# Optimization experiments

Hardware: AMD Instinct MI355X
Metric: run time of the kernel (lower is better)

Reference implementation:

```python
import math
import jax, jax.numpy as jnp
import numpy as np

HIDDEN = 2048
N_HEAD = 16
HEAD_DIM = HIDDEN // N_HEAD
LAYER_NUMBER = 1  # max(1, layer_number)
NORM_FACTOR = math.sqrt(HEAD_DIM) * LAYER_NUMBER


def build_alibi(seq_len, n_head):
    # n_head is a power of 2 -> slopes_i = 2^(-8*(i+1)/n_head)  (ALiBi paper)
    slopes = 2.0 ** (-8.0 * jnp.arange(1, n_head + 1, dtype=jnp.float32) / n_head)
    pos = jnp.arange(seq_len, dtype=jnp.float32)
    return slopes[:, None, None] * pos[None, None, :]  # (n_head, 1, seq_len)


def setup_inputs() -> dict:
    key = jax.random.key(0)
    ks = jax.random.split(key, 6)
    B, S = 2, 2048
    hidden_states = jax.random.normal(ks[0], (B, S, HIDDEN), jnp.float32)
    residual = jax.random.normal(ks[1], (B, S, HIDDEN), jnp.float32)
    attention_mask = jnp.ones((B, S), jnp.float32)  # no padding
    W_qkv = jax.random.normal(ks[2], (3 * HIDDEN, HIDDEN), jnp.float32) * (1.0 / math.sqrt(HIDDEN))
    b_qkv = jax.random.normal(ks[3], (3 * HIDDEN,), jnp.float32) * 0.02
    W_dense = jax.random.normal(ks[4], (HIDDEN, HIDDEN), jnp.float32) * (1.0 / math.sqrt(HIDDEN))
    b_dense = jax.random.normal(ks[5], (HIDDEN,), jnp.float32) * 0.02
    return {"hidden_states": hidden_states, "residual": residual,
            "attention_mask": attention_mask, "W_qkv": W_qkv, "b_qkv": b_qkv,
            "W_dense": W_dense, "b_dense": b_dense}


def reference(hidden_states, residual, attention_mask, W_qkv, b_qkv, W_dense, b_dense):
    B, S, H = hidden_states.shape
    nh, hd = N_HEAD, HEAD_DIM

    # fused QKV projection; split_tensor_along_last_dim over the per-head 3*hd axis
    mixed = hidden_states @ W_qkv.T + b_qkv              # [B,S,3H]
    mixed = mixed.reshape(B, S, nh, 3, hd)
    q = mixed[..., 0, :]                                  # [B,S,nh,hd]
    k = mixed[..., 1, :]
    v = mixed[..., 2, :]

    # baddbmm: beta*alibi + alpha*(q @ k^T)
    alibi = build_alibi(S, nh)                            # (nh,1,S)
    beta = 1.0 / LAYER_NUMBER
    alpha = 1.0 / NORM_FACTOR
    scores = alpha * jnp.einsum('bqnd,bknd->bnqk', q, k) + beta * alibi[None]  # [B,nh,S,S]

    # BloomScaledSoftmax: scale by layer_number, apply padded causal mask,
    # softmax in fp32, zero out masked probs
    scores = scores * LAYER_NUMBER
    mask_bool = attention_mask == 0.0                     # [B,S] True where padded
    causal = jnp.tril(jnp.ones((S, S), dtype=bool))       # [S,S]
    padded = (mask_bool[:, None, :, None]                 # query side
              | (~causal)[None, None]                     # causal
              | mask_bool[:, None, None, :])              # key side -> [B,1,S,S]
    scores = jnp.where(padded, jnp.float32(-10000.0), scores)
    probs = jax.nn.softmax(scores.astype(jnp.float32), axis=-1) * (~padded)
    probs = probs.astype(v.dtype)

    # attention_dropout/hidden_dropout are identity in eval mode
    context = jnp.einsum('bnqk,bknd->bqnd', probs, v).reshape(B, S, H)
    out = context @ W_dense.T + b_dense                   # dense (skip_bias_add folded)
    return residual + out
```

## Files before the change

kernel.cpp:

```cpp
#include <hip/hip_runtime.h>
#include <math.h>

#define HIDDEN 2048
#define NHEAD 16
#define HD 128
#define SEQ 2048
#define BATCH 2
#define MROWS (BATCH * SEQ)
#define K3 (3 * HIDDEN)

#define SCORE_SCALE 0.08838834764831845f

using short8 = __attribute__((ext_vector_type(8))) short;
using f32x4 = __attribute__((ext_vector_type(4))) float;

__device__ __forceinline__ unsigned short f2bf(float f) {
  union { float f; unsigned int u; } v; v.f = f;
  const unsigned int u = v.u;
  return (unsigned short)((u + 0x7FFFu + ((u >> 16) & 1u)) >> 16);
}

__device__ __forceinline__ void gl2lds16(const void* g, void* l) {
#pragma clang diagnostic push
#pragma clang diagnostic ignored "-Waddress-space-conversion"
  __builtin_amdgcn_global_load_lds(
      (const __attribute__((address_space(1))) unsigned int*)g,
      (__attribute__((address_space(3))) unsigned int*)l, 16, 0, 0);
#pragma clang diagnostic pop
}

__global__ __launch_bounds__(256) void cvt_all(
    const float* __restrict__ s0, unsigned short* __restrict__ d0, int n0,
    const float* __restrict__ s1, unsigned short* __restrict__ d1, int n1,
    const float* __restrict__ s2, unsigned short* __restrict__ d2, int n2) {
  int i = (blockIdx.x * 256 + threadIdx.x) * 8;
  const float* src;
  unsigned short* dst;
  if (i < n0) {
    src = s0; dst = d0;
  } else if (i < n0 + n1) {
    src = s1; dst = d1; i -= n0;
  } else {
    src = s2; dst = d2; i -= n0 + n1;
    if (i >= n2) return;
  }
  const float4 a = *(const float4*)(src + i);
  const float4 b = *(const float4*)(src + i + 4);
  ushort4 oa, ob;
  oa.x = f2bf(a.x); oa.y = f2bf(a.y); oa.z = f2bf(a.z); oa.w = f2bf(a.w);
  ob.x = f2bf(b.x); ob.y = f2bf(b.y); ob.z = f2bf(b.z); ob.w = f2bf(b.w);
  *(ushort4*)(dst + i) = oa;
  *(ushort4*)(dst + i + 4) = ob;
}

template <int MODE>
__global__ __launch_bounds__(256) void gemm_mfma(
    const unsigned short* __restrict__ A, const unsigned short* __restrict__ W,
    const float* __restrict__ bias, const float* __restrict__ residual,
    unsigned short* __restrict__ q, unsigned short* __restrict__ k,
    unsigned short* __restrict__ v, float* __restrict__ outf, int K) {
  __shared__ __align__(16) unsigned short As[128 * 32];
  __shared__ __align__(16) unsigned short Bs[128 * 32];
  const int tid = threadIdx.x;
  const int lane = tid & 63;
  const int wave = tid >> 6;
  const int l15 = lane & 15;
  const int quad = lane >> 4;
  const int wr = wave >> 1, wc = wave & 1;
  const int m0 = blockIdx.y << 7;
  const int n0 = blockIdx.x << 7;

  f32x4 acc[4][4];
#pragma unroll
  for (int i = 0; i < 4; ++i)
#pragma unroll
    for (int j = 0; j < 4; ++j) {
      f32x4 z = {0.f, 0.f, 0.f, 0.f};
      acc[i][j] = z;
    }

  const int kg0 = tid >> 7, mr0 = tid & 127;
  const int kg1 = (tid + 256) >> 7, mr1 = tid & 127;

  for (int k0 = 0; k0 < K; k0 += 32) {
    gl2lds16(A + (size_t)(m0 + mr0) * K + k0 + kg0 * 8, (char*)As + tid * 16);
    gl2lds16(W + (size_t)(n0 + mr0) * K + k0 + kg0 * 8, (char*)Bs + tid * 16);
    gl2lds16(A + (size_t)(m0 + mr1) * K + k0 + kg1 * 8,
             (char*)As + 4096 + tid * 16);
    gl2lds16(W + (size_t)(n0 + mr1) * K + k0 + kg1 * 8,
             (char*)Bs + 4096 + tid * 16);
    __syncthreads();
    short8 af[4], bf[4];
#pragma unroll
    for (int i = 0; i < 4; ++i)
      af[i] = *(const short8*)((const char*)As + quad * 2048 +
                               (wr * 64 + i * 16 + l15) * 16);
#pragma unroll
    for (int j = 0; j < 4; ++j)
      bf[j] = *(const short8*)((const char*)Bs + quad * 2048 +
                               (wc * 64 + j * 16 + l15) * 16);
#pragma unroll
    for (int i = 0; i < 4; ++i)
#pragma unroll
      for (int j = 0; j < 4; ++j)
        acc[i][j] =
            __builtin_amdgcn_mfma_f32_16x16x32_bf16(af[i], bf[j], acc[i][j],
                                                    0, 0, 0);
    __syncthreads();
  }

  if (MODE == 0) {
#pragma unroll
    for (int i = 0; i < 4; ++i) {
#pragma unroll
      for (int j = 0; j < 4; ++j) {
        const int n = n0 + wc * 64 + j * 16 + l15;
        const float bi = bias[n];
        const int h = n / 384;
        const int rem = n - h * 384;
        const int which = rem >> 7;
        const int d = rem & 127;
        const int mb = m0 + wr * 64 + i * 16 + quad * 4;
        const int bb = mb >> 11, ssb = mb & 2047;
        const int bh = (bb << 4) + h;
        if (which == 2) {
          const int dt = d >> 4, dl = d & 15;
          const int ksup = ssb >> 5, ntl = (ssb >> 4) & 1, qq = (ssb >> 2) & 3;
          ushort4 pk;
          pk.x = f2bf(acc[i][j][0] + bi);
          pk.y = f2bf(acc[i][j][1] + bi);
          pk.z = f2bf(acc[i][j][2] + bi);
          pk.w = f2bf(acc[i][j][3] + bi);
          *(ushort4*)(v +
                      ((((size_t)(bh * 8 + dt) * (SEQ / 32) + ksup) * 4 + qq) *
                       16 + dl) * 8 + ntl * 4) = pk;
        } else {
          unsigned short* dst = (which == 0) ? q : k;
#pragma unroll
          for (int p = 0; p < 4; ++p)
            dst[((size_t)(bh << 11) + ssb + p) * HD + d] =
                f2bf(acc[i][j][p] + bi);
        }
      }
    }
  } else {
#pragma unroll
    for (int i = 0; i < 4; ++i) {
#pragma unroll
      for (int j = 0; j < 4; ++j) {
        const int n = n0 + wc * 64 + j * 16 + l15;
        const float bi = bias[n];
#pragma unroll
        for (int p = 0; p < 4; ++p) {
          const int m = m0 + wr * 64 + i * 16 + quad * 4 + p;
          outf[(size_t)m * HIDDEN + n] =
              acc[i][j][p] + bi + residual[(size_t)m * HIDDEN + n];
        }
      }
    }
  }
}

__global__ __launch_bounds__(256) void attn_mfma3(
    const unsigned short* __restrict__ qb, const unsigned short* __restrict__ kb,
    const unsigned short* __restrict__ vt4, unsigned short* __restrict__ ctx) {
  __shared__ __align__(16) unsigned short Ks[8192];
  __shared__ __align__(16) unsigned short Vs[8192];

  const int tid = threadIdx.x;
  const int lane = tid & 63;
  const int w = tid >> 6;
  const int l15 = lane & 15;
  const int quad = lane >> 4;
  const int bt = gridDim.x - 1 - blockIdx.x;
  const int q0 = bt << 6;
  const int h = blockIdx.y, b = blockIdx.z;
  const int bh = b * NHEAD + h;
  const float slope = exp2f(-0.5f * (float)(h + 1));
  const unsigned short* qp = qb + ((size_t)bh * SEQ + q0 + w * 16) * HD;
  const unsigned short* kp = kb + (size_t)bh * SEQ * HD;
  const unsigned short* vp = vt4 + (size_t)bh * SEQ * HD;

  short8 qf[4];
#pragma unroll
  for (int dt = 0; dt < 4; ++dt)
    qf[dt] = *(const short8*)(qp + (size_t)l15 * HD + dt * 32 + quad * 8);

  f32x4 O[8];
#pragma unroll
  for (int i = 0; i < 8; ++i) {
    f32x4 z = {0.f, 0.f, 0.f, 0.f};
    O[i] = z;
  }
  float mrow = -3.0e38f, lrow = 0.f;
  const int qg = q0 + w * 16 + l15;

  for (int kt = 0; kt <= bt; ++kt) {
#pragma unroll
    for (int p = 0; p < 4; ++p) {
      const int idx = tid + p * 256;
      const int reg = idx >> 6;
      const int nts = reg >> 2, dts = reg & 3;
      const int qs = (idx >> 4) & 3, ls = idx & 15;
      gl2lds16(kp + (size_t)(kt * 64 + nts * 16 + ls) * HD + dts * 32 + qs * 8,
               (char*)Ks + idx * 16);
    }
#pragma unroll
    for (int p = 0; p < 4; ++p) {
      const int idx = tid + p * 256;
      const int ntv = idx >> 7, off = idx & 127;
      gl2lds16(vp + ((size_t)(ntv * 64 + kt * 2)) * 512 + off * 8,
               (char*)Vs + idx * 16);
    }
    __syncthreads();

    f32x4 sc[4];
#pragma unroll
    for (int nt = 0; nt < 4; ++nt) {
      f32x4 z = {0.f, 0.f, 0.f, 0.f};
      sc[nt] = z;
    }
    const int ntmax = (kt == bt) ? (w + 1) : 4;
#pragma unroll
    for (int dt = 0; dt < 4; ++dt) {
#pragma unroll
      for (int nt = 0; nt < 4; ++nt) {
        if (nt < ntmax) {
          const short8 kf = *(const short8*)(
              (const char*)Ks + ((((nt * 4 + dt) * 4 + quad) * 16 + l15) << 4));
          sc[nt] = __builtin_amdgcn_mfma_f32_16x16x32_bf16(kf, qf[dt], sc[nt],
                                                           0, 0, 0);
        }
      }
    }

    const bool diag = (kt == bt);
    float pv[4][4];
    float pm = -3.0e38f;
#pragma unroll
    for (int nt = 0; nt < 4; ++nt) {
      const int kbase = kt * 64 + nt * 16 + quad * 4;
#pragma unroll
      for (int r = 0; r < 4; ++r) {
        const int kg = kbase + r;
        float s = fmaf(sc[nt][r], SCORE_SCALE, slope * (float)kg);
        if (diag && kg > qg) s = -1.0e30f;
        pv[nt][r] = s;
        pm = fmaxf(pm, s);
      }
    }
    pm = fmaxf(pm, __shfl_xor(pm, 16, 64));
    pm = fmaxf(pm, __shfl_xor(pm, 32, 64));
    const float mnew = fmaxf(mrow, pm);
    const float alpha = __expf(mrow - mnew);
    mrow = mnew;
    float rsum = 0.f;
#pragma unroll
    for (int nt = 0; nt < 4; ++nt)
#pragma unroll
      for (int r = 0; r < 4; ++r) {
        const float p = __expf(pv[nt][r] - mnew);
        pv[nt][r] = p;
        rsum += p;
      }
    rsum += __shfl_xor(rsum, 16, 64);
    rsum += __shfl_xor(rsum, 32, 64);
    lrow = lrow * alpha + rsum;

    float aO[4];
#pragma unroll
    for (int r = 0; r < 4; ++r)
      aO[r] = __shfl(alpha, (quad << 4) + (quad << 2) + r, 64);
#pragma unroll
    for (int o = 0; o < 8; ++o)
#pragma unroll
      for (int r = 0; r < 4; ++r) O[o][r] *= aO[r];

    union { short8 s; unsigned int u[4]; } pf[2];
#pragma unroll
    for (int nt = 0; nt < 4; ++nt) {
      const unsigned int lo =
          (unsigned int)f2bf(pv[nt][0]) | ((unsigned int)f2bf(pv[nt][1]) << 16);
      const unsigned int hi =
          (unsigned int)f2bf(pv[nt][2]) | ((unsigned int)f2bf(pv[nt][3]) << 16);
      pf[nt >> 1].u[(nt & 1) * 2] = lo;
      pf[nt >> 1].u[(nt & 1) * 2 + 1] = hi;
    }

#pragma unroll
    for (int s2 = 0; s2 < 2; ++s2) {
#pragma unroll
      for (int nt = 0; nt < 8; ++nt) {
        const short8 vf = *(const short8*)(
            (const char*)Vs + nt * 2048 + s2 * 1024 + quad * 256 + l15 * 16);
        O[nt] = __builtin_amdgcn_mfma_f32_16x16x32_bf16(pf[s2].s, vf, O[nt],
                                                        0, 0, 0);
      }
    }
    __syncthreads();
  }

  const float linv = 1.f / lrow;
  float iO[4];
#pragma unroll
  for (int r = 0; r < 4; ++r)
    iO[r] = __shfl(linv, (quad << 4) + (quad << 2) + r, 64);
#pragma unroll
  for (int nt = 0; nt < 8; ++nt)
#pragma unroll
    for (int r = 0; r < 4; ++r)
      ctx[((size_t)b * SEQ + q0 + w * 16 + quad * 4 + r) * HIDDEN + h * HD +
          nt * 16 + l15] = f2bf(O[nt][r] * iO[r]);
}

extern "C" void kernel_launch(void* const* d_in, const int* in_sizes, int n_in,
                              void* d_out, int out_size, void* d_ws,
                              size_t ws_size, hipStream_t stream) {
  const float* hs = (const float*)d_in[0];
  const float* res = (const float*)d_in[1];
  const float* Wqkv = (const float*)d_in[3];
  const float* bqkv = (const float*)d_in[4];
  const float* Wd = (const float*)d_in[5];
  const float* bd = (const float*)d_in[6];
  float* out = (float*)d_out;

  const size_t per = (size_t)BATCH * NHEAD * SEQ * HD;
  const size_t n_hs = (size_t)MROWS * HIDDEN;
  const size_t n_wq = (size_t)K3 * HIDDEN;
  const size_t n_wd = (size_t)HIDDEN * HIDDEN;

  unsigned short* ws = (unsigned short*)d_ws;
  unsigned short* qb = ws;
  unsigned short* kb = qb + per;
  unsigned short* vtb = kb + per;
  unsigned short* ctxb = vtb + per;
  unsigned short* hs_bf = ctxb + n_hs;
  unsigned short* wq_bf = hs_bf + n_hs;
  unsigned short* wd_bf = wq_bf + n_wq;

  dim3 blk(256);
  const unsigned cvt_blocks = (unsigned)((n_hs + n_wq + n_wd) / 8 / 256);
  cvt_all<<<dim3(cvt_blocks), blk, 0, stream>>>(
      hs, hs_bf, (int)n_hs, Wqkv, wq_bf, (int)n_wq, Wd, wd_bf, (int)n_wd);
  gemm_mfma<0><<<dim3(K3 / 128, MROWS / 128), blk, 0, stream>>>(
      hs_bf, wq_bf, bqkv, nullptr, qb, kb, vtb, nullptr, HIDDEN);
  attn_mfma3<<<dim3(SEQ / 64, NHEAD, BATCH), blk, 0, stream>>>(qb, kb, vtb,
                                                               ctxb);
  gemm_mfma<1><<<dim3(HIDDEN / 128, MROWS / 128), blk, 0, stream>>>(
      ctxb, wd_bf, bd, res, nullptr, nullptr, nullptr, out, HIDDEN);
}
```

Baseline: 600.3 us.

## Double attention query tile per block and swizzle GEMM block order

The attention kernel now handles 128 query rows per block, with each wave owning two 16-row query subtiles. Every K/V tile loaded into LDS is therefore reused for twice as many queries, halving K/V global traffic and the number of blocks. Both GEMMs switch to a 1D grid that groups blocks into 4x4 supertiles, so neighbouring blocks share A and W tiles in L2. The costs are higher register pressure from the doubled accumulators, possibly lower occupancy, and half as many attention blocks to spread across the GPU.

```diff
diff --git a/kernel.cpp b/kernel.cpp
--- a/kernel.cpp
+++ b/kernel.cpp
@@ -53,7 +53,7 @@
   *(ushort4*)(dst + i + 4) = ob;
 }
 
-template <int MODE>
+template <int MODE, int NPN>
 __global__ __launch_bounds__(256) void gemm_mfma(
     const unsigned short* __restrict__ A, const unsigned short* __restrict__ W,
     const float* __restrict__ bias, const float* __restrict__ residual,
@@ -67,8 +67,11 @@
   const int l15 = lane & 15;
   const int quad = lane >> 4;
   const int wr = wave >> 1, wc = wave & 1;
-  const int m0 = blockIdx.y << 7;
-  const int n0 = blockIdx.x << 7;
+  const int bid = blockIdx.x;
+  const int p = bid >> 4, off = bid & 15;
+  const int pr = p / NPN, pc = p % NPN;
+  const int m0 = ((pr << 2) + (off >> 2)) << 7;
+  const int n0 = ((pc << 2) + (off & 3)) << 7;
 
   f32x4 acc[4][4];
 #pragma unroll
@@ -137,9 +140,9 @@
         } else {
           unsigned short* dst = (which == 0) ? q : k;
 #pragma unroll
-          for (int p = 0; p < 4; ++p)
-            dst[((size_t)(bh << 11) + ssb + p) * HD + d] =
-                f2bf(acc[i][j][p] + bi);
+          for (int p2 = 0; p2 < 4; ++p2)
+            dst[((size_t)(bh << 11) + ssb + p2) * HD + d] =
+                f2bf(acc[i][j][p2] + bi);
         }
       }
     }
@@ -151,17 +154,17 @@
         const int n = n0 + wc * 64 + j * 16 + l15;
         const float bi = bias[n];
 #pragma unroll
-        for (int p = 0; p < 4; ++p) {
-          const int m = m0 + wr * 64 + i * 16 + quad * 4 + p;
+        for (int p2 = 0; p2 < 4; ++p2) {
+          const int m = m0 + wr * 64 + i * 16 + quad * 4 + p2;
           outf[(size_t)m * HIDDEN + n] =
-              acc[i][j][p] + bi + residual[(size_t)m * HIDDEN + n];
-        }
-      }
-    }
-  }
-}
-
-__global__ __launch_bounds__(256) void attn_mfma3(
+              acc[i][j][p2] + bi + residual[(size_t)m * HIDDEN + n];
+        }
+      }
+    }
+  }
+}
+
+__global__ __launch_bounds__(256) void attn_mfma4(
     const unsigned short* __restrict__ qb, const unsigned short* __restrict__ kb,
     const unsigned short* __restrict__ vt4, unsigned short* __restrict__ ctx) {
   __shared__ __align__(16) unsigned short Ks[8192];
@@ -173,29 +176,37 @@
   const int l15 = lane & 15;
   const int quad = lane >> 4;
   const int bt = gridDim.x - 1 - blockIdx.x;
-  const int q0 = bt << 6;
+  const int q0 = bt << 7;
   const int h = blockIdx.y, b = blockIdx.z;
   const int bh = b * NHEAD + h;
   const float slope = exp2f(-0.5f * (float)(h + 1));
-  const unsigned short* qp = qb + ((size_t)bh * SEQ + q0 + w * 16) * HD;
+  const unsigned short* qp = qb + ((size_t)bh * SEQ + q0 + w * 32) * HD;
   const unsigned short* kp = kb + (size_t)bh * SEQ * HD;
   const unsigned short* vp = vt4 + (size_t)bh * SEQ * HD;
 
-  short8 qf[4];
+  short8 qf[4][2];
 #pragma unroll
   for (int dt = 0; dt < 4; ++dt)
-    qf[dt] = *(const short8*)(qp + (size_t)l15 * HD + dt * 32 + quad * 8);
-
-  f32x4 O[8];
+#pragma unroll
+    for (int u = 0; u < 2; ++u)
+      qf[dt][u] =
+          *(const short8*)(qp + (size_t)(u * 16 + l15) * HD + dt * 32 + quad * 8);
+
+  f32x4 O0[8], O1[8];
 #pragma unroll
   for (int i = 0; i < 8; ++i) {
     f32x4 z = {0.f, 0.f, 0.f, 0.f};
-    O[i] = z;
-  }
-  float mrow = -3.0e38f, lrow = 0.f;
-  const int qg = q0 + w * 16 + l15;
-
-  for (int kt = 0; kt <= bt; ++kt) {
+    O0[i] = z;
+    O1[i] = z;
+  }
+  float mrow0 = -3.0e38f, lrow0 = 0.f;
+  float mrow1 = -3.0e38f, lrow1 = 0.f;
+  const int qlo = q0 + w * 32;
+  const int qg0 = qlo + l15, qg1 = qlo + 16 + l15;
+  const int dlim = 2 * bt + (w >> 1);
+  const int ktend = 2 * bt + 1;
+
+  for (int kt = 0; kt <= ktend; ++kt) {
 #pragma unroll
     for (int p = 0; p < 4; ++p) {
       const int idx = tid + p * 256;
@@ -214,103 +225,143 @@
     }
     __syncthreads();
 
-    f32x4 sc[4];
-#pragma unroll
-    for (int nt = 0; nt < 4; ++nt) {
-      f32x4 z = {0.f, 0.f, 0.f, 0.f};
-      sc[nt] = z;
-    }
-    const int ntmax = (kt == bt) ? (w + 1) : 4;
-#pragma unroll
-    for (int dt = 0; dt < 4; ++dt) {
+    if (kt <= dlim) {
+      const bool diag = (kt == dlim);
+      const int ntmax = diag ? ((w & 1) ? 4 : 2) : 4;
+      const int kbase = kt << 6;
+
+      f32x4 sc0[4], sc1[4];
 #pragma unroll
       for (int nt = 0; nt < 4; ++nt) {
-        if (nt < ntmax) {
-          const short8 kf = *(const short8*)(
-              (const char*)Ks + ((((nt * 4 + dt) * 4 + quad) * 16 + l15) << 4));
-          sc[nt] = __builtin_amdgcn_mfma_f32_16x16x32_bf16(kf, qf[dt], sc[nt],
-                                                           0, 0, 0);
-        }
-      }
-    }
-
-    const bool diag = (kt == bt);
-    float pv[4][4];
-    float pm = -3.0e38f;
-#pragma unroll
-    for (int nt = 0; nt < 4; ++nt) {
-      const int kbase = kt * 64 + nt * 16 + quad * 4;
+        f32x4 z = {0.f, 0.f, 0.f, 0.f};
+        sc0[nt] = z;
+        sc1[nt] = z;
+      }
+#pragma unroll
+      for (int dt = 0; dt < 4; ++dt) {
+#pragma unroll
+        for (int nt = 0; nt < 4; ++nt) {
+          if (nt < ntmax) {
+            const short8 kf = *(const short8*)(
+                (const char*)Ks +
+                ((((nt * 4 + dt) * 4 + quad) * 16 + l15) << 4));
+            sc0[nt] = __builtin_amdgcn_mfma_f32_16x16x32_bf16(kf, qf[dt][0],
+                                                              sc0[nt], 0, 0, 0);
+            sc1[nt] = __builtin_amdgcn_mfma_f32_16x16x32_bf16(kf, qf[dt][1],
+                                                              sc1[nt], 0, 0, 0);
+          }
+        }
+      }
+
+      float pm0 = -3.0e38f, pm1 = -3.0e38f;
+#pragma unroll
+      for (int nt = 0; nt < 4; ++nt) {
+        const int kb2 = kbase + nt * 16 + quad * 4;
+#pragma unroll
+        for (int r = 0; r < 4; ++r) {
+          const int kg = kb2 + r;
+          const float ab = slope * (float)kg;
+          float s0 = fmaf(sc0[nt][r], SCORE_SCALE, ab);
+          float s1 = fmaf(sc1[nt][r], SCORE_SCALE, ab);
+          if (diag && kg > qg0) s0 = -1.0e30f;
+          if (diag && kg > qg1) s1 = -1.0e30f;
+          sc0[nt][r] = s0;
+          sc1[nt][r] = s1;
+          pm0 = fmaxf(pm0, s0);
+          pm1 = fmaxf(pm1, s1);
+        }
+      }
+      pm0 = fmaxf(pm0, __shfl_xor(pm0, 16, 64));
+      pm0 = fmaxf(pm0, __shfl_xor(pm0, 32, 64));
+      pm1 = fmaxf(pm1, __shfl_xor(pm1, 16, 64));
+      pm1 = fmaxf(pm1, __shfl_xor(pm1, 32, 64));
+      const float mn0 = fmaxf(mrow0, pm0);
+      const float mn1 = fmaxf(mrow1, pm1);
+      const float alpha0 = __expf(mrow0 - mn0);
+      const float alpha1 = __expf(mrow1 - mn1);
+      mrow0 = mn0;
+      mrow1 = mn1;
+      float rs0 = 0.f, rs1 = 0.f;
+#pragma unroll
+      for (int nt = 0; nt < 4; ++nt)
+#pragma unroll
+        for (int r = 0; r < 4; ++r) {
+          const float p0 = __expf(sc0[nt][r] - mn0);
+          const float p1 = __expf(sc1[nt][r] - mn1);
+          sc0[nt][r] = p0;
+          sc1[nt][r] = p1;
+          rs0 += p0;
+          rs1 += p1;
+        }
+      rs0 += __shfl_xor(rs0, 16, 64);
+      rs0 += __shfl_xor(rs0, 32, 64);
+      rs1 += __shfl_xor(rs1, 16, 64);
+      rs1 += __shfl_xor(rs1, 32, 64);
+      lrow0 = lrow0 * alpha0 + rs0;
+      lrow1 = lrow1 * alpha1 + rs1;
+
+      float a0[4], a1[4];
 #pragma unroll
       for (int r = 0; r < 4; ++r) {
-        const int kg = kbase + r;
-        float s = fmaf(sc[nt][r], SCORE_SCALE, slope * (float)kg);
-        if (diag && kg > qg) s = -1.0e30f;
-        pv[nt][r] = s;
-        pm = fmaxf(pm, s);
-      }
-    }
-    pm = fmaxf(pm, __shfl_xor(pm, 16, 64));
-    pm = fmaxf(pm, __shfl_xor(pm, 32, 64));
-    const float mnew = fmaxf(mrow, pm);
-    const float alpha = __expf(mrow - mnew);
-    mrow = mnew;
-    float rsum = 0.f;
-#pragma unroll
-    for (int nt = 0; nt < 4; ++nt)
-#pragma unroll
-      for (int r = 0; r < 4; ++r) {
-        const float p = __expf(pv[nt][r] - mnew);
-        pv[nt][r] = p;
-        rsum += p;
-      }
-    rsum += __shfl_xor(rsum, 16, 64);
-    rsum += __shfl_xor(rsum, 32, 64);
-    lrow = lrow * alpha + rsum;
-
-    float aO[4];
-#pragma unroll
-    for (int r = 0; r < 4; ++r)
-      aO[r] = __shfl(alpha, (quad << 4) + (quad << 2) + r, 64);
-#pragma unroll
-    for (int o = 0; o < 8; ++o)
-#pragma unroll
-      for (int r = 0; r < 4; ++r) O[o][r] *= aO[r];
-
-    union { short8 s; unsigned int u[4]; } pf[2];
-#pragma unroll
-    for (int nt = 0; nt < 4; ++nt) {
-      const unsigned int lo =
-          (unsigned int)f2bf(pv[nt][0]) | ((unsigned int)f2bf(pv[nt][1]) << 16);
-      const unsigned int hi =
-          (unsigned int)f2bf(pv[nt][2]) | ((unsigned int)f2bf(pv[nt][3]) << 16);
-      pf[nt >> 1].u[(nt & 1) * 2] = lo;
-      pf[nt >> 1].u[(nt & 1) * 2 + 1] = hi;
-    }
-
-#pragma unroll
-    for (int s2 = 0; s2 < 2; ++s2) {
-#pragma unroll
-      for (int nt = 0; nt < 8; ++nt) {
-        const short8 vf = *(const short8*)(
-            (const char*)Vs + nt * 2048 + s2 * 1024 + quad * 256 + l15 * 16);
-        O[nt] = __builtin_amdgcn_mfma_f32_16x16x32_bf16(pf[s2].s, vf, O[nt],
-                                                        0, 0, 0);
+        const int srcl = (quad << 4) + (quad << 2) + r;
+        a0[r] = __shfl(alpha0, srcl, 64);
+        a1[r] = __shfl(alpha1, srcl, 64);
+      }
+#pragma unroll
+      for (int o = 0; o < 8; ++o)
+#pragma unroll
+        for (int r = 0; r < 4; ++r) {
+          O0[o][r] *= a0[r];
+          O1[o][r] *= a1[r];
+        }
+
+      union { short8 s; unsigned int u[4]; } pf0[2], pf1[2];
+#pragma unroll
+      for (int nt = 0; nt < 4; ++nt) {
+        pf0[nt >> 1].u[(nt & 1) * 2] =
+            (unsigned int)f2bf(sc0[nt][0]) | ((unsigned int)f2bf(sc0[nt][1]) << 16);
+        pf0[nt >> 1].u[(nt & 1) * 2 + 1] =
+            (unsigned int)f2bf(sc0[nt][2]) | ((unsigned int)f2bf(sc0[nt][3]) << 16);
+        pf1[nt >> 1].u[(nt & 1) * 2] =
+            (unsigned int)f2bf(sc1[nt][0]) | ((unsigned int)f2bf(sc1[nt][1]) << 16);
+        pf1[nt >> 1].u[(nt & 1) * 2 + 1] =
+            (unsigned int)f2bf(sc1[nt][2]) | ((unsigned int)f2bf(sc1[nt][3]) << 16);
+      }
+
+#pragma unroll
+      for (int s2 = 0; s2 < 2; ++s2) {
+#pragma unroll
+        for (int nt = 0; nt < 8; ++nt) {
+          const short8 vf = *(const short8*)(
+              (const char*)Vs + nt * 2048 + s2 * 1024 + quad * 256 + l15 * 16);
+          O0[nt] = __builtin_amdgcn_mfma_f32_16x16x32_bf16(pf0[s2].s, vf,
+                                                           O0[nt], 0, 0, 0);
+          O1[nt] = __builtin_amdgcn_mfma_f32_16x16x32_bf16(pf1[s2].s, vf,
+                                                           O1[nt], 0, 0, 0);
+        }
       }
     }
     __syncthreads();
   }
 
-  const float linv = 1.f / lrow;
-  float iO[4];
-#pragma unroll
-  for (int r = 0; r < 4; ++r)
-    iO[r] = __shfl(linv, (quad << 4) + (quad << 2) + r, 64);
+  const float li0 = 1.f / lrow0;
+  const float li1 = 1.f / lrow1;
+  float i0[4], i1[4];
+#pragma unroll
+  for (int r = 0; r < 4; ++r) {
+    const int srcl = (quad << 4) + (quad << 2) + r;
+    i0[r] = __shfl(li0, srcl, 64);
+    i1[r] = __shfl(li1, srcl, 64);
+  }
 #pragma unroll
   for (int nt = 0; nt < 8; ++nt)
 #pragma unroll
-    for (int r = 0; r < 4; ++r)
-      ctx[((size_t)b * SEQ + q0 + w * 16 + quad * 4 + r) * HIDDEN + h * HD +
-          nt * 16 + l15] = f2bf(O[nt][r] * iO[r]);
+    for (int r = 0; r < 4; ++r) {
+      const size_t row = (size_t)b * SEQ + qlo + quad * 4 + r;
+      ctx[(row)*HIDDEN + h * HD + nt * 16 + l15] = f2bf(O0[nt][r] * i0[r]);
+      ctx[(row + 16) * HIDDEN + h * HD + nt * 16 + l15] =
+          f2bf(O1[nt][r] * i1[r]);
+    }
 }
 
 extern "C" void kernel_launch(void* const* d_in, const int* in_sizes, int n_in,
@@ -342,10 +393,10 @@
   const unsigned cvt_blocks = (unsigned)((n_hs + n_wq + n_wd) / 8 / 256);
   cvt_all<<<dim3(cvt_blocks), blk, 0, stream>>>(
       hs, hs_bf, (int)n_hs, Wqkv, wq_bf, (int)n_wq, Wd, wd_bf, (int)n_wd);
-  gemm_mfma<0><<<dim3(K3 / 128, MROWS / 128), blk, 0, stream>>>(
+  gemm_mfma<0, 12><<<dim3(1536), blk, 0, stream>>>(
       hs_bf, wq_bf, bqkv, nullptr, qb, kb, vtb, nullptr, HIDDEN);
-  attn_mfma3<<<dim3(SEQ / 64, NHEAD, BATCH), blk, 0, stream>>>(qb, kb, vtb,
-                                                               ctxb);
-  gemm_mfma<1><<<dim3(HIDDEN / 128, MROWS / 128), blk, 0, stream>>>(
+  attn_mfma4<<<dim3(SEQ / 128, NHEAD, BATCH), blk, 0, stream>>>(qb, kb, vtb,
+                                                                ctxb);
+  gemm_mfma<1, 4><<<dim3(512), blk, 0, stream>>>(
       ctxb, wd_bf, bd, res, nullptr, nullptr, nullptr, out, HIDDEN);
 }
```

Result: slower. 678.3 us (+13.0%).
